# Optimization experiments

Hardware: AMD Instinct MI355X
Metric: run time of the kernel (lower is better)

Reference implementation:

```python
import jax, jax.numpy as jnp
import numpy as np

N_NODES = 100000
N_EDGES = 300000
N_TYPES = 3
HID = 128
EMB = 64
N_GRAPHS = 4096
T_STEPS = 4


def setup_inputs() -> dict:
    key = jax.random.key(0)
    ks = jax.random.split(key, 12)
    s = 1.0 / np.sqrt(HID)
    return {
        "node_features": jax.random.normal(ks[0], (N_NODES, HID), jnp.float32),
        "edge_index": jax.random.randint(ks[1], (N_TYPES, 2, N_EDGES), 0, N_NODES),
        "node_to_graph_id": jnp.sort(jax.random.randint(ks[2], (N_NODES,), 0, N_GRAPHS)),
        "W_msg": jax.random.normal(ks[3], (N_TYPES, HID, HID), jnp.float32) * s,
        "b_msg": jnp.zeros((N_TYPES, HID), jnp.float32),
        "W_ih": jax.random.normal(ks[4], (3 * HID, HID), jnp.float32) * s,
        "W_hh": jax.random.normal(ks[5], (3 * HID, HID), jnp.float32) * s,
        "b_ih": jnp.zeros((3 * HID,), jnp.float32),
        "b_hh": jnp.zeros((3 * HID,), jnp.float32),
        "W_proj": jax.random.normal(ks[6], (EMB, HID), jnp.float32) * s,
        "b_proj": jnp.zeros((EMB,), jnp.float32),
        "W_gate": jax.random.normal(ks[7], (EMB, HID), jnp.float32) * s,
        "b_gate": jnp.zeros((EMB,), jnp.float32),
    }


def _gru_cell(m, h, W_ih, W_hh, b_ih, b_hh):
    # torch.nn.GRUCell math; gates ordered (r, z, n)
    gi = m @ W_ih.T + b_ih          # [N, 3H]
    gh = h @ W_hh.T + b_hh          # [N, 3H]
    i_r, i_z, i_n = jnp.split(gi, 3, axis=-1)
    h_r, h_z, h_n = jnp.split(gh, 3, axis=-1)
    r = jax.nn.sigmoid(i_r + h_r)
    z = jax.nn.sigmoid(i_z + h_z)
    n = jnp.tanh(i_n + r * h_n)
    return (1.0 - z) * n + z * h


def reference(node_features, edge_index, node_to_graph_id,
              W_msg, b_msg, W_ih, W_hh, b_ih, b_hh,
              W_proj, b_proj, W_gate, b_gate):
    h = node_features  # [N, H]

    def per_type(eidx, W, b, h):
        src, dst = eidx[0], eidx[1]
        m = h[src] @ W + b  # gather + per-edge-type linear, [E, H]
        return jax.ops.segment_sum(m, dst, num_segments=N_NODES)

    for _ in range(T_STEPS):  # fixed small T: python loop is fine
        msgs = jax.vmap(per_type, in_axes=(0, 0, 0, None))(edge_index, W_msg, b_msg, h)
        m = msgs.sum(axis=0)  # [N, H] aggregated over edge types
        h = _gru_cell(m, h, W_ih, W_hh, b_ih, b_hh)

    # gated index_add graph readout (mlp_down is identity)
    proj = h @ W_proj.T + b_proj                 # [N, E]
    gate = jax.nn.sigmoid(h @ W_gate.T + b_gate)  # [N, E]
    graph_feats = jax.ops.segment_sum(gate * proj, node_to_graph_id,
                                      num_segments=N_GRAPHS)
    return graph_feats
```

## Files before the change

### kernel.cpp

```cpp
#include <hip/hip_runtime.h>
#include <hip/hip_bf16.h>
#include <math.h>

#define NN 100000
#define NNP 100096
#define NE 300000
#define HID 128
#define EMB 64
#define NG 4096
#define DEG_CAP 32
#define XS 512

typedef __bf16 bf16x8 __attribute__((ext_vector_type(8)));
typedef float  f32x16 __attribute__((ext_vector_type(16)));
typedef short  short8 __attribute__((ext_vector_type(8)));

typedef const __attribute__((address_space(1))) unsigned int* gas_u32;
typedef __attribute__((address_space(3))) unsigned int* las_u32;

__device__ __forceinline__ void gload16(const void* g, void* l) {
    __builtin_amdgcn_global_load_lds((gas_u32)g, (las_u32)l, 16, 0, 0);
}

__device__ __forceinline__ float bf2f(unsigned short u) {
    unsigned int x = ((unsigned int)u) << 16;
    return __builtin_bit_cast(float, x);
}
__device__ __forceinline__ unsigned short f2bf(float f) {
    unsigned int x = __builtin_bit_cast(unsigned int, f);
    unsigned int r = x + 0x7fff + ((x >> 16) & 1);
    return (unsigned short)(r >> 16);
}
__device__ __forceinline__ float sigm(float x) { return 1.f / (1.f + __expf(-x)); }

__global__ __launch_bounds__(256) void k_init(const float* __restrict__ nf,
                                              unsigned short* __restrict__ X) {
    int id = blockIdx.x * 256 + threadIdx.x;
    int n = id >> 7, c = id & 127;
    X[(long)n * XS + 384 + c] = f2bf(nf[id]);
}

__global__ __launch_bounds__(256) void k_build_csr(const int* __restrict__ ei,
                                                   int* __restrict__ deg,
                                                   int* __restrict__ csr) {
    int id = blockIdx.x * 256 + threadIdx.x;
    if (id >= 3 * NE) return;
    int t = id / NE;
    int i = id - t * NE;
    int src = ei[(t * 2 + 0) * NE + i];
    int dst = ei[(t * 2 + 1) * NE + i];
    int p = atomicAdd(&deg[t * NN + dst], 1);
    if (p < DEG_CAP) csr[((long)t * NN + dst) * DEG_CAP + p] = src;
}

__global__ __launch_bounds__(256) void k_pack_deg(const int* __restrict__ deg,
                                                  int4* __restrict__ degp) {
    int n = blockIdx.x * 256 + threadIdx.x;
    if (n >= NNP) return;
    int4 v; v.x = 0; v.y = 0; v.z = 0; v.w = 0;
    if (n < NN) { v.x = deg[n]; v.y = deg[NN + n]; v.z = deg[2 * NN + n]; }
    degp[n] = v;
}

__global__ __launch_bounds__(512) void k_build_w(const float* __restrict__ Wmsg,
                                                 const float* __restrict__ Wih,
                                                 const float* __restrict__ Whh,
                                                 unsigned short* __restrict__ Wnk) {
    int n = blockIdx.x;
    int k = threadIdx.x;
    int sec = n >> 7, c = n & 127;
    float v = 0.f;
    if (k < 384) {
        if (sec < 3) {
            int t = k >> 7, kk = k & 127;
            const float* wm = Wmsg + ((long)t * HID + kk) * HID;
            const float* wi = Wih + (long)(sec * HID + c) * HID;
            float s = 0.f;
            for (int j = 0; j < HID; j++) s += wm[j] * wi[j];
            v = s;
        }
    } else {
        int kk = k - 384;
        if (sec == 0)      v = Whh[(long)c * HID + kk];
        else if (sec == 1) v = Whh[(long)(HID + c) * HID + kk];
        else if (sec == 3) v = Whh[(long)(2 * HID + c) * HID + kk];
    }
    Wnk[(long)n * 512 + k] = f2bf(v);
}

__global__ __launch_bounds__(512) void k_build_bias(const float* __restrict__ bih,
                                                    const float* __restrict__ bhh,
                                                    const float* __restrict__ bmsg,
                                                    const float* __restrict__ Wih,
                                                    float* __restrict__ bbig,
                                                    float* __restrict__ Bdeg) {
    int n = threadIdx.x;
    int sec = n >> 7, c = n & 127;
    float b;
    if (sec == 0)      b = bih[c] + bhh[c];
    else if (sec == 1) b = bih[HID + c] + bhh[HID + c];
    else if (sec == 2) b = bih[2 * HID + c];
    else               b = bhh[2 * HID + c];
    bbig[n] = b;
    for (int t = 0; t < 3; t++) {
        float s = 0.f;
        if (sec < 3) {
            const float* wi = Wih + (long)(sec * HID + c) * HID;
            const float* bm = bmsg + t * HID;
            for (int j = 0; j < HID; j++) s += bm[j] * wi[j];
        }
        Bdeg[t * 512 + n] = s;
    }
}

__global__ __launch_bounds__(256) void k_agg(unsigned short* __restrict__ X,
                                             const int* __restrict__ deg,
                                             const int* __restrict__ csr) {
    const int lane = threadIdx.x & 63;
    const long n = (long)blockIdx.x * 4 + (threadIdx.x >> 6);
    const int g = lane >> 4;
    const int c16 = lane & 15;
    const int l31 = lane & 31;

    int d[3], il[3];
#pragma unroll
    for (int t = 0; t < 3; t++) {
        int dt = deg[t * NN + n];
        d[t] = dt > DEG_CAP ? DEG_CAP : dt;
        il[t] = csr[((long)t * NN + n) * DEG_CAP + l31];
    }
#pragma unroll
    for (int t = 0; t < 3; t++) {
        float acc[8] = {0.f, 0.f, 0.f, 0.f, 0.f, 0.f, 0.f, 0.f};
        int rounds = (d[t] + 3) >> 2;
        for (int r = 0; r < rounds; r++) {
            int j = r * 4 + g;
            int idx = __shfl(il[t], j & 31);
            if (j < d[t]) {
                short8 v = *(const short8*)(X + (long)idx * XS + 384 + c16 * 8);
#pragma unroll
                for (int q = 0; q < 8; q++) acc[q] += bf2f((unsigned short)v[q]);
            }
        }
#pragma unroll
        for (int q = 0; q < 8; q++) {
            acc[q] += __shfl_xor(acc[q], 16);
            acc[q] += __shfl_xor(acc[q], 32);
        }
        if (g == 0) {
            short8 o;
#pragma unroll
            for (int q = 0; q < 8; q++) o[q] = (short)f2bf(acc[q]);
            *(short8*)(X + n * XS + t * HID + c16 * 8) = o;
        }
    }
}

__global__ __launch_bounds__(512, 2) void k_gru_mfma(
        const unsigned short* __restrict__ X, unsigned short* __restrict__ Xw,
        const unsigned short* __restrict__ Wnk,
        const float* __restrict__ bbig, const float* __restrict__ Bdeg,
        const int4* __restrict__ degp) {
    __shared__ char lds[81920];

    const int tid = threadIdx.x;
    const int lane = tid & 63;
    const int wv = tid >> 6;
    const int wr = wv >> 2;
    const int wc = wv & 3;
    const int r31 = lane & 31;
    const int kg = lane >> 5;
    const int swr = (r31 >> 1) & 3;
    const long row0 = (long)blockIdx.x * 128;

    f32x16 acc[2][4];
#pragma unroll
    for (int i = 0; i < 2; i++)
#pragma unroll
        for (int j = 0; j < 4; j++) acc[i][j] = (f32x16)(0.0f);

    const int srow = tid >> 2;
    const int su = tid & 3;
    const int swu = (su ^ ((srow >> 1) & 3)) * 16;
    const char* pA = (const char*)X + (row0 + srow) * 1024 + swu;
    const char* pB = (const char*)Wnk + (long)srow * 1024 + swu;
    const int wvb = wv * 1024;

    {
        char* Ad = &lds[wvb];
        char* Bd = &lds[8192 + wvb];
        gload16(pA, Ad);
        gload16(pB, Bd);
        gload16(pB + 131072, Bd + 8192);
        gload16(pB + 262144, Bd + 16384);
        gload16(pB + 393216, Bd + 24576);
    }

    int cur = 0;
    for (int it = 0; it < 16; it++) {
        __syncthreads();
        if (it < 15) {
            long ko = (long)(it + 1) * 64;
            char* Ad = &lds[(cur ^ 1) * 40960 + wvb];
            char* Bd = &lds[(cur ^ 1) * 40960 + 8192 + wvb];
            gload16(pA + ko, Ad);
            gload16(pB + ko, Bd);
            gload16(pB + 131072 + ko, Bd + 8192);
            gload16(pB + 262144 + ko, Bd + 16384);
            gload16(pB + 393216 + ko, Bd + 24576);
        }
        const char* Al = &lds[cur * 40960];
        const char* Bl = &lds[cur * 40960 + 8192];

        short8 af[2][2], bfr[4][2];
#pragma unroll
        for (int rt = 0; rt < 2; rt++)
#pragma unroll
            for (int kb = 0; kb < 2; kb++)
                af[rt][kb] = *(const short8*)(Al + (wr * 64 + rt * 32 + r31) * 64 +
                                              (((2 * kb + kg) ^ swr) * 16));
#pragma unroll
        for (int ct = 0; ct < 4; ct++)
#pragma unroll
            for (int kb = 0; kb < 2; kb++)
                bfr[ct][kb] = *(const short8*)(Bl + (wc * 128 + ct * 32 + r31) * 64 +
                                               (((2 * kb + kg) ^ swr) * 16));
#pragma unroll
        for (int kb = 0; kb < 2; kb++)
#pragma unroll
            for (int rt = 0; rt < 2; rt++)
#pragma unroll
                for (int ct = 0; ct < 4; ct++)
                    acc[rt][ct] = __builtin_amdgcn_mfma_f32_32x32x16_bf16(
                        __builtin_bit_cast(bf16x8, af[rt][kb]),
                        __builtin_bit_cast(bf16x8, bfr[ct][kb]),
                        acc[rt][ct], 0, 0, 0);
        cur ^= 1;
    }

    float* EX = (float*)lds;
#pragma unroll
    for (int ch = 0; ch < 8; ch++) {
        __syncthreads();
        if (wr == (ch >> 2)) {
            const int rt = (ch >> 1) & 1;
            const int half = ch & 1;
#pragma unroll
            for (int ct = 0; ct < 4; ct++) {
                int n = wc * 128 + ct * 32 + r31;
#pragma unroll
                for (int q = 0; q < 8; q++) {
                    int row16 = (q & 3) + 8 * ((q >> 2) & 1) + 4 * kg;
                    EX[row16 * 512 + n] = acc[rt][ct][half * 8 + q];
                }
            }
        }
        __syncthreads();
        {
            int row16 = tid >> 5;
            int c0 = (tid & 31) << 2;
            long grow = row0 + ch * 16 + row16;
            int4 dg = degp[grow];
            float dgx = (float)dg.x, dgy = (float)dg.y, dgz = (float)dg.z;
            const float* ex = EX + row16 * 512;
            float4 vr = *(const float4*)(ex + c0);
            float4 vz = *(const float4*)(ex + 128 + c0);
            float4 vn = *(const float4*)(ex + 256 + c0);
            float4 vh = *(const float4*)(ex + 384 + c0);
            float4 br = *(const float4*)(bbig + c0);
            float4 bz = *(const float4*)(bbig + 128 + c0);
            float4 bn = *(const float4*)(bbig + 256 + c0);
            float4 bh = *(const float4*)(bbig + 384 + c0);
            float4 d00 = *(const float4*)(Bdeg + c0);
            float4 d01 = *(const float4*)(Bdeg + 128 + c0);
            float4 d02 = *(const float4*)(Bdeg + 256 + c0);
            float4 d10 = *(const float4*)(Bdeg + 512 + c0);
            float4 d11 = *(const float4*)(Bdeg + 512 + 128 + c0);
            float4 d12 = *(const float4*)(Bdeg + 512 + 256 + c0);
            float4 d20 = *(const float4*)(Bdeg + 1024 + c0);
            float4 d21 = *(const float4*)(Bdeg + 1024 + 128 + c0);
            float4 d22 = *(const float4*)(Bdeg + 1024 + 256 + c0);
            ushort4 ho = *(const ushort4*)(X + grow * XS + 384 + c0);

            float aR[4] = {vr.x, vr.y, vr.z, vr.w};
            float aZ[4] = {vz.x, vz.y, vz.z, vz.w};
            float aN[4] = {vn.x, vn.y, vn.z, vn.w};
            float aH[4] = {vh.x, vh.y, vh.z, vh.w};
            float bR[4] = {br.x, br.y, br.z, br.w};
            float bZ[4] = {bz.x, bz.y, bz.z, bz.w};
            float bN[4] = {bn.x, bn.y, bn.z, bn.w};
            float bH[4] = {bh.x, bh.y, bh.z, bh.w};
            float e00[4] = {d00.x, d00.y, d00.z, d00.w};
            float e01[4] = {d01.x, d01.y, d01.z, d01.w};
            float e02[4] = {d02.x, d02.y, d02.z, d02.w};
            float e10[4] = {d10.x, d10.y, d10.z, d10.w};
            float e11[4] = {d11.x, d11.y, d11.z, d11.w};
            float e12[4] = {d12.x, d12.y, d12.z, d12.w};
            float e20[4] = {d20.x, d20.y, d20.z, d20.w};
            float e21[4] = {d21.x, d21.y, d21.z, d21.w};
            float e22[4] = {d22.x, d22.y, d22.z, d22.w};
            unsigned short hold[4] = {ho.x, ho.y, ho.z, ho.w};

            ushort4 outp;
            unsigned short* op = (unsigned short*)&outp;
#pragma unroll
            for (int cc = 0; cc < 4; cc++) {
                float Sr = aR[cc] + bR[cc] + dgx * e00[cc] + dgy * e10[cc] + dgz * e20[cc];
                float Sz = aZ[cc] + bZ[cc] + dgx * e01[cc] + dgy * e11[cc] + dgz * e21[cc];
                float In = aN[cc] + bN[cc] + dgx * e02[cc] + dgy * e12[cc] + dgz * e22[cc];
                float Hn = aH[cc] + bH[cc];
                float rr = sigm(Sr);
                float zz = sigm(Sz);
                float tt = In + rr * Hn;
                float e2 = __expf(2.f * tt);
                float nn = 1.f - 2.f / (e2 + 1.f);
                float hv = (1.f - zz) * nn + zz * bf2f(hold[cc]);
                op[cc] = f2bf(hv);
            }
            *(ushort4*)(Xw + grow * XS + 384 + c0) = outp;
        }
    }
}

__global__ __launch_bounds__(256) void k_readout(const unsigned short* __restrict__ X,
                                                 const int* __restrict__ n2g,
                                                 const float* __restrict__ Wp,
                                                 const float* __restrict__ bp,
                                                 const float* __restrict__ Wg,
                                                 const float* __restrict__ bg,
                                                 float* __restrict__ out) {
    __shared__ float hs[32][132];
    __shared__ float Ws[64][129];
    int tid = threadIdx.x;
    long row0 = (long)blockIdx.x * 32;
    int rg = tid >> 5, cg = tid & 31;
    float acc[4][4];
#pragma unroll
    for (int r = 0; r < 4; r++)
#pragma unroll
        for (int c = 0; c < 4; c++) acc[r][c] = 0.f;

#pragma unroll
    for (int p = 0; p < 2; p++) {
        int e = p * 256 + tid;
        int r = e >> 4, c8 = e & 15;
        short8 v = *(const short8*)(X + (row0 + r) * XS + 384 + c8 * 8);
#pragma unroll
        for (int j = 0; j < 8; j++) hs[r][c8 * 8 + j] = bf2f((unsigned short)v[j]);
    }
    for (int kc = 0; kc < 128; kc += 64) {
        __syncthreads();
#pragma unroll
        for (int p = 0; p < 8; p++) {
            int idx = p * 256 + tid;
            int j = idx >> 4, q = idx & 15;
            const float* Wsrc = (j < 64) ? Wp : Wg;
            float4 w = *(const float4*)&Wsrc[(j & 63) * HID + kc + q * 4];
            Ws[q * 4 + 0][j] = w.x;
            Ws[q * 4 + 1][j] = w.y;
            Ws[q * 4 + 2][j] = w.z;
            Ws[q * 4 + 3][j] = w.w;
        }
        __syncthreads();
#pragma unroll 8
        for (int k = 0; k < 64; k++) {
            float a[4], w[4];
#pragma unroll
            for (int r = 0; r < 4; r++) a[r] = hs[rg * 4 + r][kc + k];
#pragma unroll
            for (int c = 0; c < 4; c++) w[c] = Ws[k][cg + 32 * c];
#pragma unroll
            for (int r = 0; r < 4; r++)
#pragma unroll
                for (int c = 0; c < 4; c++) acc[r][c] += a[r] * w[c];
        }
    }
#pragma unroll
    for (int r = 0; r < 4; r++) {
        long row = row0 + rg * 4 + r;
        if (row < NN) {
            int g = n2g[row];
            float pv0 = acc[r][0] + bp[cg];
            float pv1 = acc[r][1] + bp[cg + 32];
            float gv0 = acc[r][2] + bg[cg];
            float gv1 = acc[r][3] + bg[cg + 32];
            atomicAdd(&out[g * EMB + cg],      pv0 * sigm(gv0));
            atomicAdd(&out[g * EMB + cg + 32], pv1 * sigm(gv1));
        }
    }
}

extern "C" void kernel_launch(void* const* d_in, const int* in_sizes, int n_in,
                              void* d_out, int out_size, void* d_ws, size_t ws_size,
                              hipStream_t stream) {
    const float* node_features = (const float*)d_in[0];
    const int*   edge_index    = (const int*)d_in[1];
    const int*   n2g           = (const int*)d_in[2];
    const float* W_msg         = (const float*)d_in[3];
    const float* b_msg         = (const float*)d_in[4];
    const float* W_ih          = (const float*)d_in[5];
    const float* W_hh          = (const float*)d_in[6];
    const float* b_ih          = (const float*)d_in[7];
    const float* b_hh          = (const float*)d_in[8];
    const float* W_proj        = (const float*)d_in[9];
    const float* b_proj        = (const float*)d_in[10];
    const float* W_gate        = (const float*)d_in[11];
    const float* b_gate        = (const float*)d_in[12];

    char* ws = (char*)d_ws;
    unsigned short* X    = (unsigned short*)(ws);
    unsigned short* Wnk  = (unsigned short*)(ws + 102498304);
    float*          bbig = (float*)         (ws + 103022592);
    float*          Bdeg = (float*)         (ws + 103024640);
    int4*           degp = (int4*)          (ws + 103030784);
    int*            deg  = (int*)           (ws + 104632320);
    int*            csr  = (int*)           (ws + 105832320);

    float* out = (float*)d_out;

    hipMemsetAsync(out, 0, (size_t)NG * EMB * sizeof(float), stream);
    hipMemsetAsync(deg, 0, (size_t)3 * NN * sizeof(int), stream);

    k_init<<<dim3((NN * HID) / 256), dim3(256), 0, stream>>>(node_features, X);
    k_build_csr<<<dim3((3 * NE + 255) / 256), dim3(256), 0, stream>>>(edge_index, deg, csr);
    k_pack_deg<<<dim3(NNP / 256), dim3(256), 0, stream>>>(deg, degp);
    k_build_w<<<dim3(512), dim3(512), 0, stream>>>(W_msg, W_ih, W_hh, Wnk);
    k_build_bias<<<dim3(1), dim3(512), 0, stream>>>(b_ih, b_hh, b_msg, W_ih, bbig, Bdeg);

    for (int step = 0; step < 4; step++) {
        k_agg<<<dim3(NN / 4), dim3(256), 0, stream>>>(X, deg, csr);
        k_gru_mfma<<<dim3(NNP / 128), dim3(512), 0, stream>>>(X, X, Wnk, bbig, Bdeg, degp);
    }
    k_readout<<<dim3(NN / 32), dim3(256), 0, stream>>>(X, n2g, W_proj, b_proj,
                                                       W_gate, b_gate, out);
}
```

Measured before the change: 952.2 us.

## Split hidden state into compact buffer and tile GRU GEMM over output columns

Hidden state moves out of the wide 512-column X buffer into a compact 128-column Y buffer, so edge gathers touch dense 256-byte rows instead of strided ones. Aggregation copies h into X for the GEMM input. The weight matrix is interleaved per channel (r,z,n,h gates adjacent), which lets the GRU GEMM be split into 4 column blocks of 128 with 256-thread blocks, smaller LDS and higher occupancy, each block producing 32 hidden channels. The cost is an extra h copy per step and re-reading the A tile from X in four blocks instead of one.

Result: slower. 1.003 ms (+5.4%).

```diff
diff --git a/kernel.cpp b/kernel.cpp
--- a/kernel.cpp
+++ b/kernel.cpp
@@ -34,10 +34,10 @@
 __device__ __forceinline__ float sigm(float x) { return 1.f / (1.f + __expf(-x)); }
 
 __global__ __launch_bounds__(256) void k_init(const float* __restrict__ nf,
-                                              unsigned short* __restrict__ X) {
+                                              unsigned short* __restrict__ Y) {
     int id = blockIdx.x * 256 + threadIdx.x;
     int n = id >> 7, c = id & 127;
-    X[(long)n * XS + 384 + c] = f2bf(nf[id]);
+    Y[(long)n * HID + c] = (n < NN) ? f2bf(nf[(long)n * HID + c]) : (unsigned short)0;
 }
 
 __global__ __launch_bounds__(256) void k_build_csr(const int* __restrict__ ei,
@@ -66,9 +66,9 @@
                                                  const float* __restrict__ Wih,
                                                  const float* __restrict__ Whh,
                                                  unsigned short* __restrict__ Wnk) {
-    int n = blockIdx.x;
+    int np = blockIdx.x;
     int k = threadIdx.x;
-    int sec = n >> 7, c = n & 127;
+    int c = np >> 2, sec = np & 3;
     float v = 0.f;
     if (k < 384) {
         if (sec < 3) {
@@ -85,7 +85,7 @@
         else if (sec == 1) v = Whh[(long)(HID + c) * HID + kk];
         else if (sec == 3) v = Whh[(long)(2 * HID + c) * HID + kk];
     }
-    Wnk[(long)n * 512 + k] = f2bf(v);
+    Wnk[(long)np * 512 + k] = f2bf(v);
 }
 
 __global__ __launch_bounds__(512) void k_build_bias(const float* __restrict__ bih,
@@ -94,14 +94,14 @@
                                                     const float* __restrict__ Wih,
                                                     float* __restrict__ bbig,
                                                     float* __restrict__ Bdeg) {
-    int n = threadIdx.x;
-    int sec = n >> 7, c = n & 127;
+    int np = threadIdx.x;
+    int c = np >> 2, sec = np & 3;
     float b;
     if (sec == 0)      b = bih[c] + bhh[c];
     else if (sec == 1) b = bih[HID + c] + bhh[HID + c];
     else if (sec == 2) b = bih[2 * HID + c];
     else               b = bhh[2 * HID + c];
-    bbig[n] = b;
+    bbig[np] = b;
     for (int t = 0; t < 3; t++) {
         float s = 0.f;
         if (sec < 3) {
@@ -109,11 +109,12 @@
             const float* bm = bmsg + t * HID;
             for (int j = 0; j < HID; j++) s += bm[j] * wi[j];
         }
-        Bdeg[t * 512 + n] = s;
-    }
-}
-
-__global__ __launch_bounds__(256) void k_agg(unsigned short* __restrict__ X,
+        Bdeg[t * 512 + np] = s;
+    }
+}
+
+__global__ __launch_bounds__(256) void k_agg(const unsigned short* __restrict__ Y,
+                                             unsigned short* __restrict__ X,
                                              const int* __restrict__ deg,
                                              const int* __restrict__ csr) {
     const int lane = threadIdx.x & 63;
@@ -137,7 +138,7 @@
             int j = r * 4 + g;
             int idx = __shfl(il[t], j & 31);
             if (j < d[t]) {
-                short8 v = *(const short8*)(X + (long)idx * XS + 384 + c16 * 8);
+                short8 v = *(const short8*)(Y + (long)idx * HID + c16 * 8);
 #pragma unroll
                 for (int q = 0; q < 8; q++) acc[q] += bf2f((unsigned short)v[q]);
             }
@@ -154,65 +155,68 @@
             *(short8*)(X + n * XS + t * HID + c16 * 8) = o;
         }
     }
-}
-
-__global__ __launch_bounds__(512, 2) void k_gru_mfma(
-        const unsigned short* __restrict__ X, unsigned short* __restrict__ Xw,
+    if (g == 1) {
+        short8 v = *(const short8*)(Y + n * HID + c16 * 8);
+        *(short8*)(X + n * XS + 384 + c16 * 8) = v;
+    }
+}
+
+__global__ __launch_bounds__(256, 4) void k_gru_mfma(
+        const unsigned short* __restrict__ X,
+        const unsigned short* __restrict__ Y,
+        unsigned short* __restrict__ Yw,
         const unsigned short* __restrict__ Wnk,
         const float* __restrict__ bbig, const float* __restrict__ Bdeg,
         const int4* __restrict__ degp) {
-    __shared__ char lds[81920];
+    __shared__ char lds[32768];
 
     const int tid = threadIdx.x;
     const int lane = tid & 63;
     const int wv = tid >> 6;
-    const int wr = wv >> 2;
-    const int wc = wv & 3;
+    const int wr = wv >> 1;
+    const int wc = wv & 1;
     const int r31 = lane & 31;
     const int kg = lane >> 5;
     const int swr = (r31 >> 1) & 3;
-    const long row0 = (long)blockIdx.x * 128;
-
-    f32x16 acc[2][4];
+    const int bn = blockIdx.x;
+    const long row0 = (long)blockIdx.y * 128;
+
+    f32x16 acc[2][2];
 #pragma unroll
     for (int i = 0; i < 2; i++)
 #pragma unroll
-        for (int j = 0; j < 4; j++) acc[i][j] = (f32x16)(0.0f);
-
-    const int srow = tid >> 2;
-    const int su = tid & 3;
-    const int swu = (su ^ ((srow >> 1) & 3)) * 16;
-    const char* pA = (const char*)X + (row0 + srow) * 1024 + swu;
-    const char* pB = (const char*)Wnk + (long)srow * 1024 + swu;
-    const int wvb = wv * 1024;
-
-    {
-        char* Ad = &lds[wvb];
-        char* Bd = &lds[8192 + wvb];
-        gload16(pA, Ad);
-        gload16(pB, Bd);
-        gload16(pB + 131072, Bd + 8192);
-        gload16(pB + 262144, Bd + 16384);
-        gload16(pB + 393216, Bd + 24576);
-    }
+        for (int j = 0; j < 2; j++) acc[i][j] = (f32x16)(0.0f);
+
+    const int lr = lane >> 2, su = lane & 3;
+    const int r0_ = wv * 16 + lr;
+    const int r1_ = 64 + wv * 16 + lr;
+    const char* gA0 = (const char*)X + (row0 + r0_) * 1024 + (su ^ ((r0_ >> 1) & 3)) * 16;
+    const char* gA1 = (const char*)X + (row0 + r1_) * 1024 + (su ^ ((r1_ >> 1) & 3)) * 16;
+    const char* gB0 = (const char*)Wnk + (long)(bn * 128 + r0_) * 1024 + (su ^ ((r0_ >> 1) & 3)) * 16;
+    const char* gB1 = (const char*)Wnk + (long)(bn * 128 + r1_) * 1024 + (su ^ ((r1_ >> 1) & 3)) * 16;
+    const int dst0 = (wv * 16) * 64;
+    const int dst1 = (64 + wv * 16) * 64;
+
+    gload16(gA0, lds + dst0);
+    gload16(gA1, lds + dst1);
+    gload16(gB0, lds + 8192 + dst0);
+    gload16(gB1, lds + 8192 + dst1);
 
     int cur = 0;
     for (int it = 0; it < 16; it++) {
         __syncthreads();
         if (it < 15) {
             long ko = (long)(it + 1) * 64;
-            char* Ad = &lds[(cur ^ 1) * 40960 + wvb];
-            char* Bd = &lds[(cur ^ 1) * 40960 + 8192 + wvb];
-            gload16(pA + ko, Ad);
-            gload16(pB + ko, Bd);
-            gload16(pB + 131072 + ko, Bd + 8192);
-            gload16(pB + 262144 + ko, Bd + 16384);
-            gload16(pB + 393216 + ko, Bd + 24576);
-        }
-        const char* Al = &lds[cur * 40960];
-        const char* Bl = &lds[cur * 40960 + 8192];
-
-        short8 af[2][2], bfr[4][2];
+            char* base = lds + (cur ^ 1) * 16384;
+            gload16(gA0 + ko, base + dst0);
+            gload16(gA1 + ko, base + dst1);
+            gload16(gB0 + ko, base + 8192 + dst0);
+            gload16(gB1 + ko, base + 8192 + dst1);
+        }
+        const char* Al = lds + cur * 16384;
+        const char* Bl = Al + 8192;
+
+        short8 af[2][2], bfr[2][2];
 #pragma unroll
         for (int rt = 0; rt < 2; rt++)
 #pragma unroll
@@ -220,17 +224,17 @@
                 af[rt][kb] = *(const short8*)(Al + (wr * 64 + rt * 32 + r31) * 64 +
                                               (((2 * kb + kg) ^ swr) * 16));
 #pragma unroll
-        for (int ct = 0; ct < 4; ct++)
+        for (int ct = 0; ct < 2; ct++)
 #pragma unroll
             for (int kb = 0; kb < 2; kb++)
-                bfr[ct][kb] = *(const short8*)(Bl + (wc * 128 + ct * 32 + r31) * 64 +
+                bfr[ct][kb] = *(const short8*)(Bl + (wc * 64 + ct * 32 + r31) * 64 +
                                                (((2 * kb + kg) ^ swr) * 16));
 #pragma unroll
         for (int kb = 0; kb < 2; kb++)
 #pragma unroll
             for (int rt = 0; rt < 2; rt++)
 #pragma unroll
-                for (int ct = 0; ct < 4; ct++)
+                for (int ct = 0; ct < 2; ct++)
                     acc[rt][ct] = __builtin_amdgcn_mfma_f32_32x32x16_bf16(
                         __builtin_bit_cast(bf16x8, af[rt][kb]),
                         __builtin_bit_cast(bf16x8, bfr[ct][kb]),
@@ -240,75 +244,42 @@
 
     float* EX = (float*)lds;
 #pragma unroll
-    for (int ch = 0; ch < 8; ch++) {
+    for (int band = 0; band < 4; band++) {
         __syncthreads();
-        if (wr == (ch >> 2)) {
-            const int rt = (ch >> 1) & 1;
-            const int half = ch & 1;
-#pragma unroll
-            for (int ct = 0; ct < 4; ct++) {
-                int n = wc * 128 + ct * 32 + r31;
-#pragma unroll
-                for (int q = 0; q < 8; q++) {
-                    int row16 = (q & 3) + 8 * ((q >> 2) & 1) + 4 * kg;
-                    EX[row16 * 512 + n] = acc[rt][ct][half * 8 + q];
+        if (wr == (band >> 1)) {
+            const int rt = band & 1;
+#pragma unroll
+            for (int ct = 0; ct < 2; ct++) {
+                int col = wc * 64 + ct * 32 + r31;
+#pragma unroll
+                for (int q = 0; q < 16; q++) {
+                    int rw = (q & 3) + 8 * (q >> 2) + 4 * kg;
+                    EX[rw * 132 + col] = acc[rt][ct][q];
                 }
             }
         }
         __syncthreads();
         {
-            int row16 = tid >> 5;
-            int c0 = (tid & 31) << 2;
-            long grow = row0 + ch * 16 + row16;
+            int row32 = tid >> 3, chl = tid & 7;
+            long grow = row0 + band * 32 + row32;
             int4 dg = degp[grow];
             float dgx = (float)dg.x, dgy = (float)dg.y, dgz = (float)dg.z;
-            const float* ex = EX + row16 * 512;
-            float4 vr = *(const float4*)(ex + c0);
-            float4 vz = *(const float4*)(ex + 128 + c0);
-            float4 vn = *(const float4*)(ex + 256 + c0);
-            float4 vh = *(const float4*)(ex + 384 + c0);
-            float4 br = *(const float4*)(bbig + c0);
-            float4 bz = *(const float4*)(bbig + 128 + c0);
-            float4 bn = *(const float4*)(bbig + 256 + c0);
-            float4 bh = *(const float4*)(bbig + 384 + c0);
-            float4 d00 = *(const float4*)(Bdeg + c0);
-            float4 d01 = *(const float4*)(Bdeg + 128 + c0);
-            float4 d02 = *(const float4*)(Bdeg + 256 + c0);
-            float4 d10 = *(const float4*)(Bdeg + 512 + c0);
-            float4 d11 = *(const float4*)(Bdeg + 512 + 128 + c0);
-            float4 d12 = *(const float4*)(Bdeg + 512 + 256 + c0);
-            float4 d20 = *(const float4*)(Bdeg + 1024 + c0);
-            float4 d21 = *(const float4*)(Bdeg + 1024 + 128 + c0);
-            float4 d22 = *(const float4*)(Bdeg + 1024 + 256 + c0);
-            ushort4 ho = *(const ushort4*)(X + grow * XS + 384 + c0);
-
-            float aR[4] = {vr.x, vr.y, vr.z, vr.w};
-            float aZ[4] = {vz.x, vz.y, vz.z, vz.w};
-            float aN[4] = {vn.x, vn.y, vn.z, vn.w};
-            float aH[4] = {vh.x, vh.y, vh.z, vh.w};
-            float bR[4] = {br.x, br.y, br.z, br.w};
-            float bZ[4] = {bz.x, bz.y, bz.z, bz.w};
-            float bN[4] = {bn.x, bn.y, bn.z, bn.w};
-            float bH[4] = {bh.x, bh.y, bh.z, bh.w};
-            float e00[4] = {d00.x, d00.y, d00.z, d00.w};
-            float e01[4] = {d01.x, d01.y, d01.z, d01.w};
-            float e02[4] = {d02.x, d02.y, d02.z, d02.w};
-            float e10[4] = {d10.x, d10.y, d10.z, d10.w};
-            float e11[4] = {d11.x, d11.y, d11.z, d11.w};
-            float e12[4] = {d12.x, d12.y, d12.z, d12.w};
-            float e20[4] = {d20.x, d20.y, d20.z, d20.w};
-            float e21[4] = {d21.x, d21.y, d21.z, d21.w};
-            float e22[4] = {d22.x, d22.y, d22.z, d22.w};
+            ushort4 ho = *(const ushort4*)(Y + grow * HID + bn * 32 + chl * 4);
             unsigned short hold[4] = {ho.x, ho.y, ho.z, ho.w};
-
             ushort4 outp;
             unsigned short* op = (unsigned short*)&outp;
 #pragma unroll
             for (int cc = 0; cc < 4; cc++) {
-                float Sr = aR[cc] + bR[cc] + dgx * e00[cc] + dgy * e10[cc] + dgz * e20[cc];
-                float Sz = aZ[cc] + bZ[cc] + dgx * e01[cc] + dgy * e11[cc] + dgz * e21[cc];
-                float In = aN[cc] + bN[cc] + dgx * e02[cc] + dgy * e12[cc] + dgz * e22[cc];
-                float Hn = aH[cc] + bH[cc];
+                int np = chl * 16 + cc * 4;
+                float4 v  = *(const float4*)(EX + row32 * 132 + np);
+                float4 bb = *(const float4*)(bbig + bn * 128 + np);
+                float4 b0 = *(const float4*)(Bdeg + bn * 128 + np);
+                float4 b1 = *(const float4*)(Bdeg + 512 + bn * 128 + np);
+                float4 b2 = *(const float4*)(Bdeg + 1024 + bn * 128 + np);
+                float Sr = v.x + bb.x + dgx * b0.x + dgy * b1.x + dgz * b2.x;
+                float Sz = v.y + bb.y + dgx * b0.y + dgy * b1.y + dgz * b2.y;
+                float In = v.z + bb.z + dgx * b0.z + dgy * b1.z + dgz * b2.z;
+                float Hn = v.w + bb.w;
                 float rr = sigm(Sr);
                 float zz = sigm(Sz);
                 float tt = In + rr * Hn;
@@ -317,12 +288,12 @@
                 float hv = (1.f - zz) * nn + zz * bf2f(hold[cc]);
                 op[cc] = f2bf(hv);
             }
-            *(ushort4*)(Xw + grow * XS + 384 + c0) = outp;
-        }
-    }
-}
-
-__global__ __launch_bounds__(256) void k_readout(const unsigned short* __restrict__ X,
+            *(ushort4*)(Yw + grow * HID + bn * 32 + chl * 4) = outp;
+        }
+    }
+}
+
+__global__ __launch_bounds__(256) void k_readout(const unsigned short* __restrict__ Y,
                                                  const int* __restrict__ n2g,
                                                  const float* __restrict__ Wp,
                                                  const float* __restrict__ bp,
@@ -344,7 +315,7 @@
     for (int p = 0; p < 2; p++) {
         int e = p * 256 + tid;
         int r = e >> 4, c8 = e & 15;
-        short8 v = *(const short8*)(X + (row0 + r) * XS + 384 + c8 * 8);
+        short8 v = *(const short8*)(Y + (row0 + r) * HID + c8 * 8);
 #pragma unroll
         for (int j = 0; j < 8; j++) hs[r][c8 * 8 + j] = bf2f((unsigned short)v[j]);
     }
@@ -409,28 +380,29 @@
 
     char* ws = (char*)d_ws;
     unsigned short* X    = (unsigned short*)(ws);
-    unsigned short* Wnk  = (unsigned short*)(ws + 102498304);
-    float*          bbig = (float*)         (ws + 103022592);
-    float*          Bdeg = (float*)         (ws + 103024640);
-    int4*           degp = (int4*)          (ws + 103030784);
-    int*            deg  = (int*)           (ws + 104632320);
-    int*            csr  = (int*)           (ws + 105832320);
+    unsigned short* Y    = (unsigned short*)(ws + 102498304);
+    unsigned short* Wnk  = (unsigned short*)(ws + 128122880);
+    float*          bbig = (float*)         (ws + 128647168);
+    float*          Bdeg = (float*)         (ws + 128649216);
+    int4*           degp = (int4*)          (ws + 128655360);
+    int*            deg  = (int*)           (ws + 130256896);
+    int*            csr  = (int*)           (ws + 131456896);
 
     float* out = (float*)d_out;
 
     hipMemsetAsync(out, 0, (size_t)NG * EMB * sizeof(float), stream);
     hipMemsetAsync(deg, 0, (size_t)3 * NN * sizeof(int), stream);
 
-    k_init<<<dim3((NN * HID) / 256), dim3(256), 0, stream>>>(node_features, X);
+    k_init<<<dim3((NNP * HID) / 256), dim3(256), 0, stream>>>(node_features, Y);
     k_build_csr<<<dim3((3 * NE + 255) / 256), dim3(256), 0, stream>>>(edge_index, deg, csr);
     k_pack_deg<<<dim3(NNP / 256), dim3(256), 0, stream>>>(deg, degp);
     k_build_w<<<dim3(512), dim3(512), 0, stream>>>(W_msg, W_ih, W_hh, Wnk);
     k_build_bias<<<dim3(1), dim3(512), 0, stream>>>(b_ih, b_hh, b_msg, W_ih, bbig, Bdeg);
 
     for (int step = 0; step < 4; step++) {
-        k_agg<<<dim3(NN / 4), dim3(256), 0, stream>>>(X, deg, csr);
-        k_gru_mfma<<<dim3(NNP / 128), dim3(512), 0, stream>>>(X, X, Wnk, bbig, Bdeg, degp);
-    }
-    k_readout<<<dim3(NN / 32), dim3(256), 0, stream>>>(X, n2g, W_proj, b_proj,
+        k_agg<<<dim3(NN / 4), dim3(256), 0, stream>>>(Y, X, deg, csr);
+        k_gru_mfma<<<dim3(4, NNP / 128), dim3(256), 0, stream>>>(X, Y, Y, Wnk, bbig, Bdeg, degp);
+    }
+    k_readout<<<dim3(NN / 32), dim3(256), 0, stream>>>(Y, n2g, W_proj, b_proj,
                                                        W_gate, b_gate, out);
 }
```
